# Kernel optimization log

Measured on AMD Instinct MI355X. Metric: run time of the kernel, lower is better.

The kernel has to match this reference:

```python
import jax, jax.numpy as jnp
import numpy as np

N_HEADS, N_LEVELS, N_POINTS = 8, 4, 4
D_MODEL, UNIT = 384, 128

@jax.custom_vjp
def grl(x):
    # Gradient Reversal Layer: identity forward, -grad backward (lambda_=1)
    return x

def _grl_fwd(x):
    return x, None

def _grl_bwd(res, g):
    return (-g,)

grl.defvjp(_grl_fwd, _grl_bwd)


def ms_deform_attn_core(value, spatial_shapes_np, loc, attn):
    """Multi-scale deformable attention (grid_sample bilinear, zeros padding, align_corners=False).
    value: (N, Len_in, nH, hd)   loc: (N, Lq, nH, nL, nP, 2) normalized [0,1]   attn: (N, Lq, nH, nL, nP)
    """
    N, Lq, nH, nL, nP, _ = loc.shape
    hd = value.shape[-1]
    b = jnp.arange(N).reshape(N, 1, 1, 1)
    h = jnp.arange(nH).reshape(1, 1, nH, 1)
    out = jnp.zeros((N, Lq, nH, hd), dtype=value.dtype)
    start = 0
    for l in range(nL):
        H, W = int(spatial_shapes_np[l, 0]), int(spatial_shapes_np[l, 1])
        v = value[:, start:start + H * W]  # (N, H*W, nH, hd)
        start += H * W
        # align_corners=False pixel coords
        x = loc[:, :, :, l, :, 0] * W - 0.5
        y = loc[:, :, :, l, :, 1] * H - 0.5
        x0f, y0f = jnp.floor(x), jnp.floor(y)
        lx, ly = x - x0f, y - y0f
        x0, y0 = x0f.astype(jnp.int32), y0f.astype(jnp.int32)
        def gather(xi, yi):
            valid = ((xi >= 0) & (xi < W) & (yi >= 0) & (yi < H)).astype(value.dtype)
            flat = jnp.clip(yi, 0, H - 1) * W + jnp.clip(xi, 0, W - 1)  # (N,Lq,nH,nP)
            return v[b, flat, h] * valid[..., None]  # (N,Lq,nH,nP,hd)
        s = (((1 - lx) * (1 - ly))[..., None] * gather(x0, y0)
             + (lx * (1 - ly))[..., None] * gather(x0 + 1, y0)
             + ((1 - lx) * ly)[..., None] * gather(x0, y0 + 1)
             + (lx * ly)[..., None] * gather(x0 + 1, y0 + 1))
        out = out + jnp.sum(s * attn[:, :, :, l, :, None], axis=3)
    return out.reshape(N, Lq, nH * hd)


def setup_inputs() -> dict:
    key = jax.random.key(0)
    ks = jax.random.split(key, 12)
    N, Lq = 2, 5440
    spatial = np.array([[64, 64], [32, 32], [16, 16], [8, 8]], dtype=np.int32)
    sizes = spatial[:, 0] * spatial[:, 1]
    Len_in = int(sizes.sum())  # 5440
    lsi = np.concatenate([[0], np.cumsum(sizes)[:-1]]).astype(np.int32)
    D, U, nH, nL, nP = D_MODEL, UNIT, N_HEADS, N_LEVELS, N_POINTS
    def lin(k, fin, fout):
        return jax.random.normal(k, (fin, fout), jnp.float32) / np.sqrt(fin)
    # faithful grid-init bias for sampling offsets
    thetas = np.arange(nH) * (2.0 * np.pi / nH)
    grid = np.stack([np.cos(thetas), np.sin(thetas)], -1)
    grid = grid / np.abs(grid).max(-1, keepdims=True)
    grid = np.tile(grid.reshape(nH, 1, 1, 2), (1, nL, nP, 1))
    for i in range(nP):
        grid[:, :, i, :] *= (i + 1)
    return {
        "query": jax.random.normal(ks[0], (N, Lq, D), jnp.float32),
        "reference_points": jax.random.uniform(ks[1], (N, Lq, nL, 2), jnp.float32),
        "input_flatten": jax.random.normal(ks[2], (N, Len_in, D), jnp.float32),
        "input_spatial_shapes": jnp.asarray(spatial),
        "input_level_start_index": jnp.asarray(lsi),
        "W_off": 0.01 * jax.random.normal(ks[3], (2 * U, nH * nL * nP * 2), jnp.float32),
        "b_off": jnp.asarray(grid.reshape(-1), dtype=jnp.float32),
        "W_attn": lin(ks[4], 2 * U, nH * nL * nP),
        "b_attn": jnp.zeros((nH * nL * nP,), jnp.float32),
        "W_val": lin(ks[5], 2 * U, 3 * U),
        "b_val": jnp.zeros((3 * U,), jnp.float32),
        "W_out": lin(ks[6], 3 * U, 2 * U),
        "b_out": jnp.zeros((2 * U,), jnp.float32),
        "W_attn_zd": lin(ks[7], 3 * U, nH * nL * nP),
        "b_attn_zd": jnp.zeros((nH * nL * nP,), jnp.float32),
        "W_val_zd": lin(ks[8], D, D),
        "b_val_zd": jnp.zeros((D,), jnp.float32),
        "W_out_zd": lin(ks[9], D, U),
        "b_out_zd": jnp.zeros((U,), jnp.float32),
    }


def reference(query, reference_points, input_flatten, input_spatial_shapes, input_level_start_index,
              W_off, b_off, W_attn, b_attn, W_val, b_val, W_out, b_out,
              W_attn_zd, b_attn_zd, W_val_zd, b_val_zd, W_out_zd, b_out_zd):
    N, Lq, _ = query.shape
    nH, nL, nP, U = N_HEADS, N_LEVELS, N_POINTS, UNIT
    ss = np.asarray(input_spatial_shapes)  # static level shapes
    sample_query = query[..., :2 * U]
    off = (sample_query @ W_off + b_off).reshape(N, Lq, nH, nL, nP, 2)
    # offset normalizer = [W_l, H_l] per level
    norm = jnp.asarray(np.stack([ss[:, 1], ss[:, 0]], -1), dtype=query.dtype)
    loc = reference_points[:, :, None, :, None, :] + off / norm[None, None, None, :, None, :]
    # top (content) path
    top_val = (input_flatten[..., :2 * U] @ W_val + b_val).reshape(N, -1, nH, 3 * U // nH)
    aw = jax.nn.softmax((sample_query @ W_attn + b_attn).reshape(N, Lq, nH, nL * nP), -1)
    aw = aw.reshape(N, Lq, nH, nL, nP)
    top_out = ms_deform_attn_core(top_val, ss, loc, aw) @ W_out + b_out
    # bottom (domain) path with gradient reversal on content slice
    bot_val_in = jnp.concatenate([grl(input_flatten[..., :2 * U]), input_flatten[..., 2 * U:]], -1)
    bot_val = (bot_val_in @ W_val_zd + b_val_zd).reshape(N, -1, nH, D_MODEL // nH)
    bot_query = jnp.concatenate([grl(query[..., :2 * U]), query[..., 2 * U:]], -1)
    aw_zd = jax.nn.softmax((bot_query @ W_attn_zd + b_attn_zd).reshape(N, Lq, nH, nL * nP), -1)
    aw_zd = aw_zd.reshape(N, Lq, nH, nL, nP)
    bot_out = ms_deform_attn_core(bot_val, ss, loc, aw_zd) @ W_out_zd + b_out_zd
    return jnp.concatenate([top_out, bot_out], -1)
```

## Files before the change

### kernel.cpp

```cpp
#include <hip/hip_runtime.h>
#include <hip/hip_bf16.h>
#include <math.h>

#define DM   384
#define U2   256
#define HD   48

typedef __attribute__((ext_vector_type(8))) short short8;
typedef __attribute__((ext_vector_type(4))) float floatx4;

static __device__ __forceinline__ unsigned short f2bfbits(float f) {
    __hip_bfloat16 h = __float2bfloat16(f);
    return *reinterpret_cast<unsigned short*>(&h);
}
static __device__ __forceinline__ unsigned pack2(float x, float y) {
    return (unsigned)f2bfbits(x) | ((unsigned)f2bfbits(y) << 16);
}
static __device__ __forceinline__ float bflo(unsigned u) { return __uint_as_float(u << 16); }
static __device__ __forceinline__ float bfhi(unsigned u) { return __uint_as_float(u & 0xffff0000u); }

#define GLDS16(g, l)  __builtin_amdgcn_global_load_lds(                        \
    (const __attribute__((address_space(1))) unsigned int*)(g),                \
    (__attribute__((address_space(3))) unsigned int*)(l), 16, 0, 0)

struct PrepParams {
    const float* q; const float* f;
    __hip_bfloat16 *q_bf, *f_bf;
    const float* wsrc[7]; __hip_bfloat16* wdst[7];
    int K[7], N[7], off[8];
    int nQ4, nF4, total;
};
__global__ __launch_bounds__(256) void prep_kernel(PrepParams d) {
    const int idx = blockIdx.x * 256 + threadIdx.x;
    if (idx >= d.total) return;
    if (idx < d.nQ4) {
        const int i4 = idx * 4;
        const float4 v = *(const float4*)&d.q[i4];
        uint2 pk; pk.x = pack2(v.x, v.y); pk.y = pack2(v.z, v.w);
        *(uint2*)&d.q_bf[i4] = pk;
        return;
    }
    if (idx < d.nQ4 + d.nF4) {
        const int i4 = (idx - d.nQ4) * 4;
        const float4 v = *(const float4*)&d.f[i4];
        uint2 pk; pk.x = pack2(v.x, v.y); pk.y = pack2(v.z, v.w);
        *(uint2*)&d.f_bf[i4] = pk;
        return;
    }
    const int iw = idx - d.nQ4 - d.nF4;
    int s = 0;
#pragma unroll
    for (int i = 1; i < 7; ++i) if (iw >= d.off[i]) s = i;
    const int r = iw - d.off[s];
    const int k = r / d.N[s], n = r - k * d.N[s];
    d.wdst[s][(size_t)n * d.K[s] + k] = __float2bfloat16(d.wsrc[s][r]);
}

struct Seg {
    const __hip_bfloat16* A; int lda;
    const __hip_bfloat16* Bt; int ldbt;
    const float* bias; void* C; int ldc; int K; int omode;
};
struct SegParams { Seg seg[5]; int ystart[5]; int nseg; };

__global__ __launch_bounds__(256) void gemm_seg_kernel(SegParams p) {
    __shared__ __hip_bfloat16 As[128 * 32];
    __shared__ __hip_bfloat16 Bs[128 * 32];

    const int yb = blockIdx.y;
    int s = 0;
#pragma unroll
    for (int i = 1; i < 5; ++i) if (i < p.nseg && yb >= p.ystart[i]) s = i;
    Seg sg;
    switch (s) {
        case 0: sg = p.seg[0]; break;
        case 1: sg = p.seg[1]; break;
        case 2: sg = p.seg[2]; break;
        case 3: sg = p.seg[3]; break;
        default: sg = p.seg[4]; break;
    }
    const int by = yb - p.ystart[s];

    const int t    = threadIdx.x;
    const int bm   = blockIdx.x * 128;
    const int bn   = by * 128;
    const int w    = t >> 6, lane = t & 63;
    const int wm   = (w >> 1) * 64, wn = (w & 1) * 64;
    const int quad = lane >> 4, lm = lane & 15;

    const int sr = lane >> 2;
    const int pc = lane & 3;
    const int r0loc = 32 * w + sr;
    const int r1loc = r0loc + 16;
    const int c0 = pc ^ ((r0loc >> 1) & 3);
    const int c1 = pc ^ ((r1loc >> 1) & 3);

    const __hip_bfloat16* Ag0 = sg.A  + (size_t)(bm + r0loc) * sg.lda  + c0 * 8;
    const __hip_bfloat16* Ag1 = sg.A  + (size_t)(bm + r1loc) * sg.lda  + c1 * 8;
    const __hip_bfloat16* Bg0 = sg.Bt + (size_t)(bn + r0loc) * sg.ldbt + c0 * 8;
    const __hip_bfloat16* Bg1 = sg.Bt + (size_t)(bn + r1loc) * sg.ldbt + c1 * 8;
    __hip_bfloat16* Al0 = As + (32 * w) * 32;
    __hip_bfloat16* Al1 = As + (32 * w + 16) * 32;
    __hip_bfloat16* Bl0 = Bs + (32 * w) * 32;
    __hip_bfloat16* Bl1 = Bs + (32 * w + 16) * 32;

    floatx4 acc[4][4] = {};

    for (int k0 = 0; k0 < sg.K; k0 += 32) {
        GLDS16(Ag0 + k0, Al0);
        GLDS16(Ag1 + k0, Al1);
        GLDS16(Bg0 + k0, Bl0);
        GLDS16(Bg1 + k0, Bl1);
        __syncthreads();

        short8 af[4], bf[4];
#pragma unroll
        for (int i = 0; i < 4; ++i) {
            const int row = wm + i * 16 + lm;
            af[i] = *(const short8*)&As[row * 32 + ((quad ^ ((row >> 1) & 3)) * 8)];
        }
#pragma unroll
        for (int j = 0; j < 4; ++j) {
            const int row = wn + j * 16 + lm;
            bf[j] = *(const short8*)&Bs[row * 32 + ((quad ^ ((row >> 1) & 3)) * 8)];
        }
#pragma unroll
        for (int i = 0; i < 4; ++i)
#pragma unroll
            for (int j = 0; j < 4; ++j)
                acc[i][j] = __builtin_amdgcn_mfma_f32_16x16x32_bf16(
                    af[i], bf[j], acc[i][j], 0, 0, 0);
        __syncthreads();
    }

#pragma unroll
    for (int i = 0; i < 4; ++i)
#pragma unroll
        for (int reg = 0; reg < 4; ++reg) {
            const int row = bm + wm + i * 16 + quad * 4 + reg;
#pragma unroll
            for (int j = 0; j < 4; ++j) {
                const int col = bn + wn + j * 16 + lm;
                const float v = acc[i][j][reg] + sg.bias[col];
                if (sg.omode == 0) {
                    ((float*)sg.C)[(size_t)row * sg.ldc + col] = v;
                } else if (sg.omode == 1) {
                    ((__hip_bfloat16*)sg.C)[(size_t)row * sg.ldc + col] = __float2bfloat16(v);
                } else {
                    const int h = col / 48;
                    const size_t idx = (size_t)row * 768 + h * 96 +
                                       ((sg.omode == 3) ? 48 : 0) + (col - h * 48);
                    ((__hip_bfloat16*)sg.C)[idx] = __float2bfloat16(v);
                }
            }
        }
}

#define SPP 524

__global__ __launch_bounds__(192) void sampler_kernel(
    const float* __restrict__ off_buf,
    const float* __restrict__ logit_top,
    const float* __restrict__ logit_bot,
    const float* __restrict__ ref_pts,
    const int*   __restrict__ ss,
    const int*   __restrict__ lsi,
    const __hip_bfloat16* __restrict__ vcomb,
    __hip_bfloat16* __restrict__ core_top,
    __hip_bfloat16* __restrict__ core_bot,
    int Lq, int LenIn)
{
    __shared__ float    sA[4][128];
    __shared__ unsigned sP[4][SPP];

    const int bid = blockIdx.x;
    const int Q0  = bid * 2;
    const int t   = threadIdx.x;

    float gw[2][4];
    int   gp[2][4];
#pragma unroll
    for (int slot = 0; slot < 2; ++slot) {
        const bool active = slot ? (t >= 64) : (t < 128);
        if (!active) continue;
        const int qL = slot;
        const int e  = slot ? (t - 64) : t;
        const int gq = Q0 + qL;
        const int n  = gq / Lq;
        const int l  = (e >> 2) & 3;
        const float2 offv = *(const float2*)&off_buf[(size_t)gq * 256 + 2 * e];
        const float rx = ref_pts[(size_t)(gq * 4 + l) * 2 + 0];
        const float ry = ref_pts[(size_t)(gq * 4 + l) * 2 + 1];
        const int H = ss[2 * l], W = ss[2 * l + 1];
        const int start = lsi[l];

        const float x = (rx + offv.x / (float)W) * (float)W - 0.5f;
        const float y = (ry + offv.y / (float)H) * (float)H - 0.5f;
        const float x0f = floorf(x), y0f = floorf(y);
        const float lx = x - x0f, ly = y - y0f;
        const int ix0 = (int)x0f, iy0 = (int)y0f;
        const int ix1 = ix0 + 1,  iy1 = iy0 + 1;

        const float vx0 = (ix0 >= 0 && ix0 < W) ? 1.f : 0.f;
        const float vx1 = (ix1 >= 0 && ix1 < W) ? 1.f : 0.f;
        const float vy0 = (iy0 >= 0 && iy0 < H) ? 1.f : 0.f;
        const float vy1 = (iy1 >= 0 && iy1 < H) ? 1.f : 0.f;
        const int cx0 = min(max(ix0, 0), W - 1);
        const int cx1 = min(max(ix1, 0), W - 1);
        const int cy0 = min(max(iy0, 0), H - 1);
        const int cy1 = min(max(iy1, 0), H - 1);
        const int base = n * LenIn + start;

        gp[slot][0] = base + cy0 * W + cx0;
        gp[slot][1] = base + cy0 * W + cx1;
        gp[slot][2] = base + cy1 * W + cx0;
        gp[slot][3] = base + cy1 * W + cx1;
        gw[slot][0] = (1.f - lx) * (1.f - ly) * vx0 * vy0;
        gw[slot][1] = lx * (1.f - ly) * vx1 * vy0;
        gw[slot][2] = (1.f - lx) * ly * vx0 * vy1;
        gw[slot][3] = lx * ly * vx1 * vy1;
    }

    if (t < 32) {
        const int q  = t >> 4;
        const int br = (t >> 3) & 1;
        const int h  = t & 7;
        const float* L = (br ? logit_bot : logit_top) + (size_t)(Q0 + q) * 128 + h * 16;
        float lg[16];
        *(float4*)&lg[0]  = *(const float4*)&L[0];
        *(float4*)&lg[4]  = *(const float4*)&L[4];
        *(float4*)&lg[8]  = *(const float4*)&L[8];
        *(float4*)&lg[12] = *(const float4*)&L[12];
        float m = -1e30f;
#pragma unroll
        for (int j = 0; j < 16; ++j) m = fmaxf(m, lg[j]);
        float ex[16], sum = 0.f;
#pragma unroll
        for (int j = 0; j < 16; ++j) { ex[j] = expf(lg[j] - m); sum += ex[j]; }
        const float inv = 1.f / sum;
#pragma unroll
        for (int j = 0; j < 16; ++j) sA[q * 2 + br][h * 16 + j] = ex[j] * inv;
    }
    __syncthreads();

#pragma unroll
    for (int slot = 0; slot < 2; ++slot) {
        const bool active = slot ? (t >= 64) : (t < 128);
        if (!active) continue;
        const int e = slot ? (t - 64) : t;
        const int pidx = 4 * e + (e >> 4);
#pragma unroll
        for (int br = 0; br < 2; ++br) {
            const float a = sA[slot * 2 + br][e];
#pragma unroll
            for (int k = 0; k < 4; ++k) {
                sP[slot * 2 + br][pidx + k] =
                    ((unsigned)f2bfbits(gw[slot][k] * a) << 16) | (unsigned)gp[slot][k];
            }
        }
    }
    __syncthreads();

    const int q  = t / 96;
    const int r  = t - q * 96;
    const int g  = r / 6;
    const int m  = r - g * 6;
    const int br = g & 1;
    const int h  = g >> 1;

    const unsigned* P = sP[q * 2 + br];
    const char* vb = (const char*)vcomb + h * 192 + br * 96 + m * 16;

    float a0 = 0.f, a1 = 0.f, a2 = 0.f, a3 = 0.f;
    float a4 = 0.f, a5 = 0.f, a6 = 0.f, a7 = 0.f;
#pragma unroll 4
    for (int lp = 0; lp < 16; ++lp) {
        const int ib = 65 * h + 4 * lp;
#pragma unroll
        for (int k = 0; k < 4; ++k) {
            const unsigned u = P[ib + k];
            const float wv = __uint_as_float(u & 0xffff0000u);
            const unsigned pt = u & 0x3fffu;
            const uint4 v = *(const uint4*)(vb + pt * 1536u);
            a0 = fmaf(wv, bflo(v.x), a0);
            a1 = fmaf(wv, bfhi(v.x), a1);
            a2 = fmaf(wv, bflo(v.y), a2);
            a3 = fmaf(wv, bfhi(v.y), a3);
            a4 = fmaf(wv, bflo(v.z), a4);
            a5 = fmaf(wv, bfhi(v.z), a5);
            a6 = fmaf(wv, bflo(v.w), a6);
            a7 = fmaf(wv, bfhi(v.w), a7);
        }
    }
    uint4 o;
    o.x = pack2(a0, a1); o.y = pack2(a2, a3);
    o.z = pack2(a4, a5); o.w = pack2(a6, a7);
    __hip_bfloat16* dst = br ? core_bot : core_top;
    *(uint4*)&dst[(size_t)(Q0 + q) * DM + h * HD + m * 8] = o;
}

extern "C" void kernel_launch(void* const* d_in, const int* in_sizes, int n_in,
                              void* d_out, int out_size, void* d_ws, size_t ws_size,
                              hipStream_t stream) {
    const float* query   = (const float*)d_in[0];
    const float* refpts  = (const float*)d_in[1];
    const float* flat    = (const float*)d_in[2];
    const int*   ss      = (const int*)d_in[3];
    const int*   lsi     = (const int*)d_in[4];
    const float* W_off   = (const float*)d_in[5];
    const float* b_off   = (const float*)d_in[6];
    const float* W_attn  = (const float*)d_in[7];
    const float* b_attn  = (const float*)d_in[8];
    const float* W_val   = (const float*)d_in[9];
    const float* b_val   = (const float*)d_in[10];
    const float* W_out   = (const float*)d_in[11];
    const float* b_out   = (const float*)d_in[12];
    const float* W_attn_zd = (const float*)d_in[13];
    const float* b_attn_zd = (const float*)d_in[14];
    const float* W_val_zd  = (const float*)d_in[15];
    const float* b_val_zd  = (const float*)d_in[16];
    const float* W_out_zd  = (const float*)d_in[17];
    const float* b_out_zd  = (const float*)d_in[18];

    const int Lq    = in_sizes[0] / (2 * DM);
    const int LenIn = in_sizes[2] / (2 * DM);
    const int M  = 2 * Lq;
    const int Mv = 2 * LenIn;

    float* out = (float*)d_out;

    float* ws      = (float*)d_ws;
    float* off_buf = ws;
    float* lt      = off_buf + (size_t)M * 256;
    float* lb      = lt + (size_t)M * 128;
    __hip_bfloat16* q_bf  = (__hip_bfloat16*)(lb + (size_t)M * 128);
    __hip_bfloat16* f_bf  = q_bf + (size_t)M * 384;
    __hip_bfloat16* vcomb = f_bf + (size_t)Mv * 384;
    __hip_bfloat16* ct    = vcomb + (size_t)Mv * 768;
    __hip_bfloat16* cb    = ct + (size_t)M * 384;
    __hip_bfloat16* wtb   = cb + (size_t)M * 384;

    PrepParams pp;
    pp.q = query; pp.f = flat;
    pp.q_bf = q_bf; pp.f_bf = f_bf;
    const float* srcs[7] = {W_attn, W_attn_zd, W_val, W_val_zd, W_out, W_out_zd, W_off};
    const int Ks[7] = {256, 384, 256, 384, 384, 384, 256};
    const int Ns[7] = {128, 128, 384, 384, 256, 128, 256};
    __hip_bfloat16* dsts[7];
    int off = 0;
    for (int i = 0; i < 7; ++i) {
        pp.wsrc[i] = srcs[i]; pp.K[i] = Ks[i]; pp.N[i] = Ns[i];
        pp.off[i] = off;
        dsts[i] = wtb + off;
        pp.wdst[i] = dsts[i];
        off += Ks[i] * Ns[i];
    }
    pp.off[7] = off;
    pp.nQ4 = M * DM / 4;
    pp.nF4 = Mv * DM / 4;
    pp.total = pp.nQ4 + pp.nF4 + off;

    const dim3 blk(256);
    const int mg = M / 128;

    prep_kernel<<<dim3((pp.total + 255) / 256), blk, 0, stream>>>(pp);

    {
        SegParams p;
        p.seg[0] = { q_bf, DM, dsts[6], 256, b_off,    off_buf, 256, 256, 0 };
        p.seg[1] = { q_bf, DM, dsts[0], 256, b_attn,   lt,      128, 256, 0 };
        p.seg[2] = { q_bf, DM, dsts[1], 384, b_attn_zd,lb,      128, 384, 0 };
        p.seg[3] = { f_bf, DM, dsts[2], 256, b_val,    vcomb,   0,   256, 2 };
        p.seg[4] = { f_bf, DM, dsts[3], 384, b_val_zd, vcomb,   0,   384, 3 };
        p.ystart[0] = 0; p.ystart[1] = 2; p.ystart[2] = 3;
        p.ystart[3] = 4; p.ystart[4] = 7;
        p.nseg = 5;
        gemm_seg_kernel<<<dim3(mg, 10), blk, 0, stream>>>(p);
    }

    sampler_kernel<<<dim3(M / 2), dim3(192), 0, stream>>>(
        off_buf, lt, lb, refpts, ss, lsi, vcomb, ct, cb, Lq, LenIn);

    {
        SegParams p;
        p.seg[0] = { ct, DM, dsts[4], 384, b_out,    out,      DM, 384, 0 };
        p.seg[1] = { cb, DM, dsts[5], 384, b_out_zd, out + U2, DM, 384, 0 };
        p.ystart[0] = 0; p.ystart[1] = 2;
        p.nseg = 2;
        gemm_seg_kernel<<<dim3(mg, 3), blk, 0, stream>>>(p);
    }
}
```

Measured before the change: 253.5 us.

## Fuse fp32-to-bf16 conversion of inputs and weights into GEMM tile loads

```diff
diff --git a/kernel.cpp b/kernel.cpp
--- a/kernel.cpp
+++ b/kernel.cpp
@@ -19,46 +19,9 @@
 static __device__ __forceinline__ float bflo(unsigned u) { return __uint_as_float(u << 16); }
 static __device__ __forceinline__ float bfhi(unsigned u) { return __uint_as_float(u & 0xffff0000u); }
 
-#define GLDS16(g, l)  __builtin_amdgcn_global_load_lds(                        \
-    (const __attribute__((address_space(1))) unsigned int*)(g),                \
-    (__attribute__((address_space(3))) unsigned int*)(l), 16, 0, 0)
-
-struct PrepParams {
-    const float* q; const float* f;
-    __hip_bfloat16 *q_bf, *f_bf;
-    const float* wsrc[7]; __hip_bfloat16* wdst[7];
-    int K[7], N[7], off[8];
-    int nQ4, nF4, total;
-};
-__global__ __launch_bounds__(256) void prep_kernel(PrepParams d) {
-    const int idx = blockIdx.x * 256 + threadIdx.x;
-    if (idx >= d.total) return;
-    if (idx < d.nQ4) {
-        const int i4 = idx * 4;
-        const float4 v = *(const float4*)&d.q[i4];
-        uint2 pk; pk.x = pack2(v.x, v.y); pk.y = pack2(v.z, v.w);
-        *(uint2*)&d.q_bf[i4] = pk;
-        return;
-    }
-    if (idx < d.nQ4 + d.nF4) {
-        const int i4 = (idx - d.nQ4) * 4;
-        const float4 v = *(const float4*)&d.f[i4];
-        uint2 pk; pk.x = pack2(v.x, v.y); pk.y = pack2(v.z, v.w);
-        *(uint2*)&d.f_bf[i4] = pk;
-        return;
-    }
-    const int iw = idx - d.nQ4 - d.nF4;
-    int s = 0;
-#pragma unroll
-    for (int i = 1; i < 7; ++i) if (iw >= d.off[i]) s = i;
-    const int r = iw - d.off[s];
-    const int k = r / d.N[s], n = r - k * d.N[s];
-    d.wdst[s][(size_t)n * d.K[s] + k] = __float2bfloat16(d.wsrc[s][r]);
-}
-
 struct Seg {
-    const __hip_bfloat16* A; int lda;
-    const __hip_bfloat16* Bt; int ldbt;
+    const void* A; int lda; int aty;
+    const float* W; int ldw;
     const float* bias; void* C; int ldc; int K; int omode;
 };
 struct SegParams { Seg seg[5]; int ystart[5]; int nseg; };
@@ -88,29 +51,49 @@
     const int wm   = (w >> 1) * 64, wn = (w & 1) * 64;
     const int quad = lane >> 4, lm = lane & 15;
 
-    const int sr = lane >> 2;
-    const int pc = lane & 3;
-    const int r0loc = 32 * w + sr;
-    const int r1loc = r0loc + 16;
-    const int c0 = pc ^ ((r0loc >> 1) & 3);
-    const int c1 = pc ^ ((r1loc >> 1) & 3);
-
-    const __hip_bfloat16* Ag0 = sg.A  + (size_t)(bm + r0loc) * sg.lda  + c0 * 8;
-    const __hip_bfloat16* Ag1 = sg.A  + (size_t)(bm + r1loc) * sg.lda  + c1 * 8;
-    const __hip_bfloat16* Bg0 = sg.Bt + (size_t)(bn + r0loc) * sg.ldbt + c0 * 8;
-    const __hip_bfloat16* Bg1 = sg.Bt + (size_t)(bn + r1loc) * sg.ldbt + c1 * 8;
-    __hip_bfloat16* Al0 = As + (32 * w) * 32;
-    __hip_bfloat16* Al1 = As + (32 * w + 16) * 32;
-    __hip_bfloat16* Bl0 = Bs + (32 * w) * 32;
-    __hip_bfloat16* Bl1 = Bs + (32 * w + 16) * 32;
+    const int arow = t >> 1, ahalf = t & 1;
+    const int ac0 = (ahalf * 2)     ^ ((arow >> 1) & 3);
+    const int ac1 = (ahalf * 2 + 1) ^ ((arow >> 1) & 3);
+    const int bn_ = t & 127, bkh = t >> 7;
+    const int bc0 = (bkh * 2)     ^ ((bn_ >> 1) & 3);
+    const int bc1 = (bkh * 2 + 1) ^ ((bn_ >> 1) & 3);
 
     floatx4 acc[4][4] = {};
 
     for (int k0 = 0; k0 < sg.K; k0 += 32) {
-        GLDS16(Ag0 + k0, Al0);
-        GLDS16(Ag1 + k0, Al1);
-        GLDS16(Bg0 + k0, Bl0);
-        GLDS16(Bg1 + k0, Bl1);
+        if (sg.aty) {
+            const __hip_bfloat16* src = (const __hip_bfloat16*)sg.A +
+                (size_t)(bm + arow) * sg.lda + k0 + ahalf * 16;
+            *(short8*)&As[arow * 32 + ac0 * 8] = *(const short8*)src;
+            *(short8*)&As[arow * 32 + ac1 * 8] = *(const short8*)(src + 8);
+        } else {
+            const float* src = (const float*)sg.A +
+                (size_t)(bm + arow) * sg.lda + k0 + ahalf * 16;
+            const float4 f0 = *(const float4*)(src + 0);
+            const float4 f1 = *(const float4*)(src + 4);
+            const float4 f2 = *(const float4*)(src + 8);
+            const float4 f3 = *(const float4*)(src + 12);
+            uint4 lo, hi;
+            lo.x = pack2(f0.x, f0.y); lo.y = pack2(f0.z, f0.w);
+            lo.z = pack2(f1.x, f1.y); lo.w = pack2(f1.z, f1.w);
+            hi.x = pack2(f2.x, f2.y); hi.y = pack2(f2.z, f2.w);
+            hi.z = pack2(f3.x, f3.y); hi.w = pack2(f3.z, f3.w);
+            *(uint4*)&As[arow * 32 + ac0 * 8] = lo;
+            *(uint4*)&As[arow * 32 + ac1 * 8] = hi;
+        }
+        {
+            const float* wsrc = sg.W + (size_t)(k0 + bkh * 16) * sg.ldw + bn + bn_;
+            float v[16];
+#pragma unroll
+            for (int i = 0; i < 16; ++i) v[i] = wsrc[(size_t)i * sg.ldw];
+            uint4 lo, hi;
+            lo.x = pack2(v[0], v[1]);  lo.y = pack2(v[2], v[3]);
+            lo.z = pack2(v[4], v[5]);  lo.w = pack2(v[6], v[7]);
+            hi.x = pack2(v[8], v[9]);  hi.y = pack2(v[10], v[11]);
+            hi.z = pack2(v[12], v[13]); hi.w = pack2(v[14], v[15]);
+            *(uint4*)&Bs[bn_ * 32 + bc0 * 8] = lo;
+            *(uint4*)&Bs[bn_ * 32 + bc1 * 8] = hi;
+        }
         __syncthreads();
 
         short8 af[4], bf[4];
@@ -333,45 +316,20 @@
     float* off_buf = ws;
     float* lt      = off_buf + (size_t)M * 256;
     float* lb      = lt + (size_t)M * 128;
-    __hip_bfloat16* q_bf  = (__hip_bfloat16*)(lb + (size_t)M * 128);
-    __hip_bfloat16* f_bf  = q_bf + (size_t)M * 384;
-    __hip_bfloat16* vcomb = f_bf + (size_t)Mv * 384;
+    __hip_bfloat16* vcomb = (__hip_bfloat16*)(lb + (size_t)M * 128);
     __hip_bfloat16* ct    = vcomb + (size_t)Mv * 768;
     __hip_bfloat16* cb    = ct + (size_t)M * 384;
-    __hip_bfloat16* wtb   = cb + (size_t)M * 384;
-
-    PrepParams pp;
-    pp.q = query; pp.f = flat;
-    pp.q_bf = q_bf; pp.f_bf = f_bf;
-    const float* srcs[7] = {W_attn, W_attn_zd, W_val, W_val_zd, W_out, W_out_zd, W_off};
-    const int Ks[7] = {256, 384, 256, 384, 384, 384, 256};
-    const int Ns[7] = {128, 128, 384, 384, 256, 128, 256};
-    __hip_bfloat16* dsts[7];
-    int off = 0;
-    for (int i = 0; i < 7; ++i) {
-        pp.wsrc[i] = srcs[i]; pp.K[i] = Ks[i]; pp.N[i] = Ns[i];
-        pp.off[i] = off;
-        dsts[i] = wtb + off;
-        pp.wdst[i] = dsts[i];
-        off += Ks[i] * Ns[i];
-    }
-    pp.off[7] = off;
-    pp.nQ4 = M * DM / 4;
-    pp.nF4 = Mv * DM / 4;
-    pp.total = pp.nQ4 + pp.nF4 + off;
 
     const dim3 blk(256);
     const int mg = M / 128;
 
-    prep_kernel<<<dim3((pp.total + 255) / 256), blk, 0, stream>>>(pp);
-
     {
         SegParams p;
-        p.seg[0] = { q_bf, DM, dsts[6], 256, b_off,    off_buf, 256, 256, 0 };
-        p.seg[1] = { q_bf, DM, dsts[0], 256, b_attn,   lt,      128, 256, 0 };
-        p.seg[2] = { q_bf, DM, dsts[1], 384, b_attn_zd,lb,      128, 384, 0 };
-        p.seg[3] = { f_bf, DM, dsts[2], 256, b_val,    vcomb,   0,   256, 2 };
-        p.seg[4] = { f_bf, DM, dsts[3], 384, b_val_zd, vcomb,   0,   384, 3 };
+        p.seg[0] = { query, DM, 0, W_off,     256, b_off,     off_buf, 256, 256, 0 };
+        p.seg[1] = { query, DM, 0, W_attn,    128, b_attn,    lt,      128, 256, 0 };
+        p.seg[2] = { query, DM, 0, W_attn_zd, 128, b_attn_zd, lb,      128, 384, 0 };
+        p.seg[3] = { flat,  DM, 0, W_val,     384, b_val,     vcomb,   0,   256, 2 };
+        p.seg[4] = { flat,  DM, 0, W_val_zd,  384, b_val_zd,  vcomb,   0,   384, 3 };
         p.ystart[0] = 0; p.ystart[1] = 2; p.ystart[2] = 3;
         p.ystart[3] = 4; p.ystart[4] = 7;
         p.nseg = 5;
@@ -383,8 +341,8 @@
 
     {
         SegParams p;
-        p.seg[0] = { ct, DM, dsts[4], 384, b_out,    out,      DM, 384, 0 };
-        p.seg[1] = { cb, DM, dsts[5], 384, b_out_zd, out + U2, DM, 384, 0 };
+        p.seg[0] = { ct, DM, 1, W_out,    256, b_out,    out,      DM, 384, 0 };
+        p.seg[1] = { cb, DM, 1, W_out_zd, 128, b_out_zd, out + U2, DM, 384, 0 };
         p.ystart[0] = 0; p.ystart[1] = 2;
         p.nseg = 2;
         gemm_seg_kernel<<<dim3(mg, 3), blk, 0, stream>>>(p);
```

Result: no change. 256.9 us (+1.4%).
